# Optimization experiments

Hardware: AMD Instinct MI355X
Metric: run time of the kernel (lower is better)

## Reference

```python
import jax, jax.numpy as jnp
import numpy as np

D = 256  # atom_feature_dim
LN_EPS = 1e-5
NEG_SLOPE = 0.01  # LeakyReLU default


def setup_inputs() -> dict:
    key = jax.random.key(0)
    ks = jax.random.split(key, 8)
    B, N, L = 16, 256, 1024
    inv = 1.0 / np.sqrt(D)
    return {
        "mol_atom_feature": jax.random.normal(ks[0], (B, N, D), jnp.float32),
        "atom_feature": jax.random.normal(ks[1], (B, L, D), jnp.float32),
        "mol_atom_attend_mask": jnp.ones((B, L), jnp.float32),
        "mol_atom_softmax_mask": jnp.zeros((B, L), jnp.float32),
        # nn.Linear(D, D) params (weight stored [out, in] torch-style; we use x @ W.T form via einsum)
        "W_mol": jax.random.uniform(ks[2], (D, D), jnp.float32, -inv, inv),
        "b_mol": jnp.zeros((D,), jnp.float32),
        "W_nb": jax.random.uniform(ks[3], (D, D), jnp.float32, -inv, inv),
        "b_nb": jnp.zeros((D,), jnp.float32),
        # nn.Linear(2D, 1): weight [2D], bias scalar
        "align_w": jax.random.uniform(ks[4], (2 * D,), jnp.float32, -1.0 / np.sqrt(2 * D), 1.0 / np.sqrt(2 * D)),
        "align_b": jnp.zeros((), jnp.float32),
        "ln_gamma": jnp.ones((D,), jnp.float32),
        "ln_beta": jnp.zeros((D,), jnp.float32),
    }


def reference(mol_atom_feature, atom_feature, mol_atom_attend_mask, mol_atom_softmax_mask,
              W_mol, b_mol, W_nb, b_nb, align_w, align_b, ln_gamma, ln_beta):
    # Linear transforms (dropout is identity in eval)
    x = jnp.einsum('bnd,ed->bne', mol_atom_feature, W_mol) + b_mol   # [B,N,D]
    a = jnp.einsum('bld,ed->ble', atom_feature, W_nb) + b_nb        # [B,L,D]

    # GAT align: Linear over concat([x_i, a_j]) is separable:
    # score[b,n,l] = x[b,n]@w1 + a[b,l]@w2 + b
    w1, w2 = align_w[:D], align_w[D:]
    score = (x @ w1)[:, :, None] + (a @ w2)[:, None, :] + align_b   # [B,N,L]
    score = jax.nn.leaky_relu(score, NEG_SLOPE)

    # additive softmax mask over atom axis, then masked softmax + attend mask
    score = score + mol_atom_softmax_mask[:, None, :]
    attn = jax.nn.softmax(score, axis=-1)
    attn = attn * mol_atom_attend_mask[:, None, :]

    # weighted aggregation of transformed atom features
    ctx = jnp.einsum('bnl,bld->bnd', attn, a)                        # [B,N,D]

    # LayerNorm
    mu = jnp.mean(ctx, axis=-1, keepdims=True)
    var = jnp.var(ctx, axis=-1, keepdims=True)
    out = (ctx - mu) * jax.lax.rsqrt(var + LN_EPS) * ln_gamma + ln_beta
    return out
```

## Files before the change

### kernel.cpp

```cpp
#include <hip/hip_runtime.h>
#include <hip/hip_bf16.h>
#include <math.h>

#define BB 16
#define NN 256
#define LL 1024
#define DD 256

constexpr float LN_EPS = 1e-5f;
constexpr float NEG_SLOPE = 0.01f;

typedef __attribute__((ext_vector_type(8))) short short8;
typedef __attribute__((ext_vector_type(4))) float f32x4;
typedef __attribute__((ext_vector_type(4))) int i32x4;

static __device__ __forceinline__ unsigned cvtpk(float lo, float hi) {
  __hip_bfloat162 h = __float22bfloat162_rn(make_float2(lo, hi));
  union { __hip_bfloat162 h; unsigned u; } v; v.h = h;
  return v.u;
}
static __device__ __forceinline__ short8 pack8(float4 f0, float4 f1) {
  union { i32x4 i; short8 s; } v;
  v.i.x = cvtpk(f0.x, f0.y);
  v.i.y = cvtpk(f0.z, f0.w);
  v.i.z = cvtpk(f1.x, f1.y);
  v.i.w = cvtpk(f1.z, f1.w);
  return v.s;
}
static __device__ __forceinline__ unsigned short f2bf(float f) {
  union { float f; unsigned u; } v; v.f = f;
  unsigned r = v.u + 0x7FFFu + ((v.u >> 16) & 1u);
  return (unsigned short)(r >> 16);
}
static __device__ __forceinline__ float bf2f(unsigned short u) {
  union { unsigned u; float f; } v; v.u = ((unsigned)u) << 16;
  return v.f;
}

__global__ __launch_bounds__(512) void agemm_kernel(
    const float* __restrict__ atom, const float* __restrict__ W_nb,
    const float* __restrict__ b_nb, const float* __restrict__ W_mol,
    const float* __restrict__ b_mol, const float* __restrict__ align_w,
    const float* __restrict__ align_b, unsigned short* __restrict__ aT,
    float* __restrict__ s2, float* __restrict__ v1c) {
  __shared__ char atile[64 * 256 * 2];
  __shared__ unsigned short sAT[256 * 68];
  __shared__ float vp[32][16];

  int t = threadIdx.x;
  int w = t >> 6, lane = t & 63;
  int i = blockIdx.x;
  int x = i & 7, k = i >> 3;
  int b = x + 8 * (k >> 4);
  int l0 = (k & 15) * 64;
  int lo16 = lane & 15, g = lane >> 4;

  {
    int r = t >> 3, dseg = (t & 7) * 32;
    const float* src = atom + (size_t)(b * LL + l0 + r) * DD + dseg;
    #pragma unroll
    for (int q = 0; q < 4; ++q) {
      float4 f0 = *(const float4*)(src + q * 8);
      float4 f1 = *(const float4*)(src + q * 8 + 4);
      int byte = ((r * 256 + dseg + q * 8) * 2) ^ ((r & 7) << 4);
      *(short8*)(atile + byte) = pack8(f0, f1);
    }
  }

  if (i < 16) {
    int d0 = i * 16;
    int dl = t & 15, eseg = t >> 4;
    float acc = 0.f;
    #pragma unroll
    for (int q = 0; q < 8; ++q) {
      int e = eseg * 8 + q;
      acc += align_w[e] * W_mol[e * DD + d0 + dl];
    }
    vp[eseg][dl] = acc;
    __syncthreads();
    if (t < 16) {
      float s = 0.f;
      #pragma unroll
      for (int q = 0; q < 32; ++q) s += vp[q][t];
      v1c[d0 + t] = s;
    }
    if (i == 0 && w == 1) {
      float s = b_mol[lane] * align_w[lane] +
                b_mol[lane + 64] * align_w[lane + 64] +
                b_mol[lane + 128] * align_w[lane + 128] +
                b_mol[lane + 192] * align_w[lane + 192];
      #pragma unroll
      for (int off = 32; off > 0; off >>= 1) s += __shfl_xor(s, off, 64);
      if (lane == 0) v1c[256] = s + align_b[0];
    }
  }
  __syncthreads();

  f32x4 acc[2][4];
  #pragma unroll
  for (int m = 0; m < 2; ++m)
    #pragma unroll
    for (int n = 0; n < 4; ++n) acc[m][n] = f32x4{0.f, 0.f, 0.f, 0.f};

  const float* Ap = W_nb + (size_t)(w * 32 + lo16) * DD + g * 8;

  #pragma unroll 2
  for (int kk = 0; kk < 8; ++kk) {
    short8 af[2];
    #pragma unroll
    for (int m = 0; m < 2; ++m) {
      float4 f0 = *(const float4*)(Ap + m * 16 * DD + kk * 32);
      float4 f1 = *(const float4*)(Ap + m * 16 * DD + kk * 32 + 4);
      af[m] = pack8(f0, f1);
    }
    short8 bf[4];
    #pragma unroll
    for (int n = 0; n < 4; ++n) {
      int l = n * 16 + lo16;
      int byte = ((l * 256 + kk * 32 + g * 8) * 2) ^ ((l & 7) << 4);
      bf[n] = *(const short8*)(atile + byte);
    }
    #pragma unroll
    for (int m = 0; m < 2; ++m)
      #pragma unroll
      for (int n = 0; n < 4; ++n)
        acc[m][n] = __builtin_amdgcn_mfma_f32_16x16x32_bf16(af[m], bf[n],
                                                            acc[m][n], 0, 0, 0);
  }

  #pragma unroll
  for (int m = 0; m < 2; ++m) {
    int e_lo = w * 32 + m * 16 + g * 4;
    float4 bias = *(const float4*)&b_nb[e_lo];
    #pragma unroll
    for (int n = 0; n < 4; ++n) {
      int l = n * 16 + lo16;
      #pragma unroll
      for (int j = 0; j < 4; ++j) {
        float v = acc[m][n][j] + ((const float*)&bias)[j];
        sAT[(e_lo + j) * 68 + l] = f2bf(v);
      }
    }
  }
  __syncthreads();

  {
    int l = t >> 3, ech = (t & 7) * 32;
    float s = 0.f;
    #pragma unroll 8
    for (int q = 0; q < 32; ++q) {
      int e = ech + q;
      s += align_w[DD + e] * bf2f(sAT[e * 68 + l]);
    }
    s += __shfl_xor(s, 1, 64);
    s += __shfl_xor(s, 2, 64);
    s += __shfl_xor(s, 4, 64);
    if ((t & 7) == 0) s2[b * LL + l0 + l] = s;
  }

  unsigned short* dst = aT + (size_t)b * DD * LL + l0;
  #pragma unroll
  for (int idx = t; idx < 4096; idx += 512) {
    int e = idx >> 4, ch = idx & 15;
    ushort4 v = *(const ushort4*)&sAT[e * 68 + ch * 4];
    *(ushort4*)(dst + (size_t)e * LL + ch * 4) = v;
  }
}

__global__ __launch_bounds__(512) void attn_kernel(
    const unsigned short* __restrict__ aT, const float* __restrict__ mol,
    const float* __restrict__ v1c, const float* __restrict__ s2,
    const float* __restrict__ amask, const float* __restrict__ smask,
    const float* __restrict__ gamma, const float* __restrict__ beta,
    float* __restrict__ out) {
  __shared__ unsigned short sattn[16 * 1024];
  __shared__ float ctxp[2][16][DD];
  __shared__ float v1s[256];
  __shared__ float s1s[16];
  __shared__ float mu_s[16], rs_s[16];
  int i = blockIdx.x;
  int x = i & 7, k = i >> 3;
  int b = x + 8 * (k >> 4);
  int n0 = (k & 15) * 16;
  int t = threadIdx.x, w = t >> 6, lane = t & 63;

  float c0 = v1c[256];
  if (t < 256) v1s[t] = v1c[t];
  __syncthreads();

  {
    int r = t >> 5, off = (t & 31) * 8;
    const float* mr = mol + (size_t)(b * NN + n0 + r) * DD + off;
    float s = 0.f;
    #pragma unroll
    for (int q = 0; q < 2; ++q) {
      float4 f = *(const float4*)(mr + q * 4);
      s += f.x * v1s[off + q * 4] + f.y * v1s[off + q * 4 + 1] +
           f.z * v1s[off + q * 4 + 2] + f.w * v1s[off + q * 4 + 3];
    }
    s += __shfl_xor(s, 1, 64);
    s += __shfl_xor(s, 2, 64);
    s += __shfl_xor(s, 4, 64);
    s += __shfl_xor(s, 8, 64);
    s += __shfl_xor(s, 16, 64);
    if ((t & 31) == 0) s1s[r] = s + c0;
  }
  __syncthreads();

  {
    float s2v[16], amv[16], smv[16];
    #pragma unroll
    for (int q = 0; q < 16; ++q) {
      int l = lane + 64 * q;
      s2v[q] = s2[b * LL + l];
      amv[q] = amask[b * LL + l];
      smv[q] = smask[b * LL + l];
    }
    #pragma unroll
    for (int rr = 0; rr < 2; ++rr) {
      int r = w * 2 + rr;
      float s1v = s1s[r];
      float p[16];
      float mx = -INFINITY;
      #pragma unroll
      for (int q = 0; q < 16; ++q) {
        float sc = s1v + s2v[q];
        sc = sc > 0.f ? sc : NEG_SLOPE * sc;
        sc += smv[q];
        p[q] = sc;
        mx = fmaxf(mx, sc);
      }
      #pragma unroll
      for (int off = 32; off > 0; off >>= 1) mx = fmaxf(mx, __shfl_xor(mx, off, 64));
      float sum = 0.f;
      #pragma unroll
      for (int q = 0; q < 16; ++q) {
        p[q] = __expf(p[q] - mx);
        sum += p[q];
      }
      #pragma unroll
      for (int off = 32; off > 0; off >>= 1) sum += __shfl_xor(sum, off, 64);
      float inv = 1.f / sum;
      #pragma unroll
      for (int q = 0; q < 16; ++q) {
        unsigned short bv = f2bf(p[q] * amv[q] * inv);
        int l = lane + 64 * q;
        int byte = ((r * 1024 + l) * 2) ^ ((r & 7) << 4);
        *(unsigned short*)((char*)sattn + byte) = bv;
      }
    }
  }
  __syncthreads();

  int lo16 = lane & 15, g = lane >> 4;
  int e0 = (w & 3) * 64, lh = w >> 2;
  f32x4 acc[4];
  #pragma unroll
  for (int n = 0; n < 4; ++n) acc[n] = f32x4{0.f, 0.f, 0.f, 0.f};
  const unsigned short* Bp =
      aT + (size_t)b * DD * LL + (size_t)(e0 + lo16) * LL + lh * 512 + g * 8;
  #pragma unroll 4
  for (int kk = 0; kk < 16; ++kk) {
    short8 afr = *(const short8*)((const char*)sattn +
        (((lo16 * 1024 + lh * 512 + kk * 32 + g * 8) * 2) ^ ((lo16 & 7) << 4)));
    #pragma unroll
    for (int n = 0; n < 4; ++n) {
      short8 bfr = *(const short8*)(Bp + (size_t)n * 16 * LL + kk * 32);
      acc[n] = __builtin_amdgcn_mfma_f32_16x16x32_bf16(afr, bfr, acc[n], 0, 0, 0);
    }
  }
  #pragma unroll
  for (int n = 0; n < 4; ++n)
    #pragma unroll
    for (int j = 0; j < 4; ++j)
      ctxp[lh][g * 4 + j][e0 + n * 16 + lo16] = acc[n][j];
  __syncthreads();

  #pragma unroll
  for (int rr = 0; rr < 2; ++rr) {
    int r = w * 2 + rr;
    float s = 0.f, sq = 0.f;
    #pragma unroll
    for (int jj = 0; jj < 4; ++jj) {
      int cc = lane + 64 * jj;
      float v = ctxp[0][r][cc] + ctxp[1][r][cc];
      s += v;
      sq += v * v;
    }
    #pragma unroll
    for (int off = 32; off > 0; off >>= 1) {
      s += __shfl_xor(s, off, 64);
      sq += __shfl_xor(sq, off, 64);
    }
    if (lane == 0) {
      float mu = s * (1.f / 256.f);
      float var = sq * (1.f / 256.f) - mu * mu;
      mu_s[r] = mu;
      rs_s[r] = rsqrtf(var + LN_EPS);
    }
  }
  __syncthreads();

  #pragma unroll
  for (int q = 0; q < 8; ++q) {
    int idx = t + 512 * q;
    int r = idx >> 8, d = idx & 255;
    float v = ctxp[0][r][d] + ctxp[1][r][d];
    out[(size_t)(b * NN + n0 + r) * DD + d] =
        (v - mu_s[r]) * rs_s[r] * gamma[d] + beta[d];
  }
}

extern "C" void kernel_launch(void* const* d_in, const int* in_sizes, int n_in,
                              void* d_out, int out_size, void* d_ws, size_t ws_size,
                              hipStream_t stream) {
  const float* mol     = (const float*)d_in[0];
  const float* atom    = (const float*)d_in[1];
  const float* amask   = (const float*)d_in[2];
  const float* smask   = (const float*)d_in[3];
  const float* W_mol   = (const float*)d_in[4];
  const float* b_mol   = (const float*)d_in[5];
  const float* W_nb    = (const float*)d_in[6];
  const float* b_nb    = (const float*)d_in[7];
  const float* align_w = (const float*)d_in[8];
  const float* align_b = (const float*)d_in[9];
  const float* gamma   = (const float*)d_in[10];
  const float* beta    = (const float*)d_in[11];
  float* outp = (float*)d_out;

  char* wsb = (char*)d_ws;
  unsigned short* aT = (unsigned short*)wsb;
  float* s2  = (float*)(wsb + 8388608);
  float* v1c = s2 + BB * LL;

  agemm_kernel<<<256, 512, 0, stream>>>(atom, W_nb, b_nb, W_mol, b_mol,
                                        align_w, align_b, aT, s2, v1c);
  attn_kernel<<<256, 512, 0, stream>>>(aT, mol, v1c, s2, amask, smask,
                                       gamma, beta, outp);
}
```

Before: 40.79 us.

## Double threads per block to 1024 and redistribute work in both kernels

Both kernels now launch 1024 threads (16 waves) per block instead of 512. Each wave handles half as much work: in the GEMM each wave owns one 16-row M tile, and in the attention kernel each wave owns one softmax row and a quarter of the L reduction, with four partial ctx buffers summed afterwards. The goal is more waves per CU to hide memory latency on a grid of only 256 blocks. In exchange, shared memory grows for ctxp, the partial sums need an extra reduction step, and per-thread register limits get tighter.

Result: slower. 41.66 us (+2.1%).

```diff
diff --git a/kernel.cpp b/kernel.cpp
--- a/kernel.cpp
+++ b/kernel.cpp
@@ -37,7 +37,7 @@
   return v.f;
 }
 
-__global__ __launch_bounds__(512) void agemm_kernel(
+__global__ __launch_bounds__(1024) void agemm_kernel(
     const float* __restrict__ atom, const float* __restrict__ W_nb,
     const float* __restrict__ b_nb, const float* __restrict__ W_mol,
     const float* __restrict__ b_mol, const float* __restrict__ align_w,
@@ -45,7 +45,7 @@
     float* __restrict__ s2, float* __restrict__ v1c) {
   __shared__ char atile[64 * 256 * 2];
   __shared__ unsigned short sAT[256 * 68];
-  __shared__ float vp[32][16];
+  __shared__ float vp[64][16];
 
   int t = threadIdx.x;
   int w = t >> 6, lane = t & 63;
@@ -56,10 +56,10 @@
   int lo16 = lane & 15, g = lane >> 4;
 
   {
-    int r = t >> 3, dseg = (t & 7) * 32;
+    int r = t >> 4, dseg = (t & 15) * 16;
     const float* src = atom + (size_t)(b * LL + l0 + r) * DD + dseg;
     #pragma unroll
-    for (int q = 0; q < 4; ++q) {
+    for (int q = 0; q < 2; ++q) {
       float4 f0 = *(const float4*)(src + q * 8);
       float4 f1 = *(const float4*)(src + q * 8 + 4);
       int byte = ((r * 256 + dseg + q * 8) * 2) ^ ((r & 7) << 4);
@@ -72,8 +72,8 @@
     int dl = t & 15, eseg = t >> 4;
     float acc = 0.f;
     #pragma unroll
-    for (int q = 0; q < 8; ++q) {
-      int e = eseg * 8 + q;
+    for (int q = 0; q < 4; ++q) {
+      int e = eseg * 4 + q;
       acc += align_w[e] * W_mol[e * DD + d0 + dl];
     }
     vp[eseg][dl] = acc;
@@ -81,7 +81,7 @@
     if (t < 16) {
       float s = 0.f;
       #pragma unroll
-      for (int q = 0; q < 32; ++q) s += vp[q][t];
+      for (int q = 0; q < 64; ++q) s += vp[q][t];
       v1c[d0 + t] = s;
     }
     if (i == 0 && w == 1) {
@@ -96,48 +96,35 @@
   }
   __syncthreads();
 
-  f32x4 acc[2][4];
-  #pragma unroll
-  for (int m = 0; m < 2; ++m)
-    #pragma unroll
-    for (int n = 0; n < 4; ++n) acc[m][n] = f32x4{0.f, 0.f, 0.f, 0.f};
-
-  const float* Ap = W_nb + (size_t)(w * 32 + lo16) * DD + g * 8;
-
-  #pragma unroll 2
+  f32x4 acc[4];
+  #pragma unroll
+  for (int n = 0; n < 4; ++n) acc[n] = f32x4{0.f, 0.f, 0.f, 0.f};
+
+  const float* Ap = W_nb + (size_t)(w * 16 + lo16) * DD + g * 8;
+
+  #pragma unroll 4
   for (int kk = 0; kk < 8; ++kk) {
-    short8 af[2];
-    #pragma unroll
-    for (int m = 0; m < 2; ++m) {
-      float4 f0 = *(const float4*)(Ap + m * 16 * DD + kk * 32);
-      float4 f1 = *(const float4*)(Ap + m * 16 * DD + kk * 32 + 4);
-      af[m] = pack8(f0, f1);
-    }
-    short8 bf[4];
+    float4 f0 = *(const float4*)(Ap + kk * 32);
+    float4 f1 = *(const float4*)(Ap + kk * 32 + 4);
+    short8 af = pack8(f0, f1);
     #pragma unroll
     for (int n = 0; n < 4; ++n) {
       int l = n * 16 + lo16;
       int byte = ((l * 256 + kk * 32 + g * 8) * 2) ^ ((l & 7) << 4);
-      bf[n] = *(const short8*)(atile + byte);
-    }
-    #pragma unroll
-    for (int m = 0; m < 2; ++m)
-      #pragma unroll
-      for (int n = 0; n < 4; ++n)
-        acc[m][n] = __builtin_amdgcn_mfma_f32_16x16x32_bf16(af[m], bf[n],
-                                                            acc[m][n], 0, 0, 0);
-  }
-
-  #pragma unroll
-  for (int m = 0; m < 2; ++m) {
-    int e_lo = w * 32 + m * 16 + g * 4;
+      short8 bf = *(const short8*)(atile + byte);
+      acc[n] = __builtin_amdgcn_mfma_f32_16x16x32_bf16(af, bf, acc[n], 0, 0, 0);
+    }
+  }
+
+  {
+    int e_lo = w * 16 + g * 4;
     float4 bias = *(const float4*)&b_nb[e_lo];
     #pragma unroll
     for (int n = 0; n < 4; ++n) {
       int l = n * 16 + lo16;
       #pragma unroll
       for (int j = 0; j < 4; ++j) {
-        float v = acc[m][n][j] + ((const float*)&bias)[j];
+        float v = acc[n][j] + ((const float*)&bias)[j];
         sAT[(e_lo + j) * 68 + l] = f2bf(v);
       }
     }
@@ -145,36 +132,37 @@
   __syncthreads();
 
   {
-    int l = t >> 3, ech = (t & 7) * 32;
+    int l = t >> 4, ech = (t & 15) * 16;
     float s = 0.f;
     #pragma unroll 8
-    for (int q = 0; q < 32; ++q) {
+    for (int q = 0; q < 16; ++q) {
       int e = ech + q;
       s += align_w[DD + e] * bf2f(sAT[e * 68 + l]);
     }
     s += __shfl_xor(s, 1, 64);
     s += __shfl_xor(s, 2, 64);
     s += __shfl_xor(s, 4, 64);
-    if ((t & 7) == 0) s2[b * LL + l0 + l] = s;
+    s += __shfl_xor(s, 8, 64);
+    if ((t & 15) == 0) s2[b * LL + l0 + l] = s;
   }
 
   unsigned short* dst = aT + (size_t)b * DD * LL + l0;
   #pragma unroll
-  for (int idx = t; idx < 4096; idx += 512) {
+  for (int idx = t; idx < 4096; idx += 1024) {
     int e = idx >> 4, ch = idx & 15;
     ushort4 v = *(const ushort4*)&sAT[e * 68 + ch * 4];
     *(ushort4*)(dst + (size_t)e * LL + ch * 4) = v;
   }
 }
 
-__global__ __launch_bounds__(512) void attn_kernel(
+__global__ __launch_bounds__(1024) void attn_kernel(
     const unsigned short* __restrict__ aT, const float* __restrict__ mol,
     const float* __restrict__ v1c, const float* __restrict__ s2,
     const float* __restrict__ amask, const float* __restrict__ smask,
     const float* __restrict__ gamma, const float* __restrict__ beta,
     float* __restrict__ out) {
   __shared__ unsigned short sattn[16 * 1024];
-  __shared__ float ctxp[2][16][DD];
+  __shared__ float ctxp[4][16][DD];
   __shared__ float v1s[256];
   __shared__ float s1s[16];
   __shared__ float mu_s[16], rs_s[16];
@@ -189,80 +177,63 @@
   __syncthreads();
 
   {
-    int r = t >> 5, off = (t & 31) * 8;
-    const float* mr = mol + (size_t)(b * NN + n0 + r) * DD + off;
-    float s = 0.f;
-    #pragma unroll
-    for (int q = 0; q < 2; ++q) {
-      float4 f = *(const float4*)(mr + q * 4);
-      s += f.x * v1s[off + q * 4] + f.y * v1s[off + q * 4 + 1] +
-           f.z * v1s[off + q * 4 + 2] + f.w * v1s[off + q * 4 + 3];
-    }
-    s += __shfl_xor(s, 1, 64);
-    s += __shfl_xor(s, 2, 64);
-    s += __shfl_xor(s, 4, 64);
-    s += __shfl_xor(s, 8, 64);
-    s += __shfl_xor(s, 16, 64);
-    if ((t & 31) == 0) s1s[r] = s + c0;
-  }
-  __syncthreads();
-
-  {
-    float s2v[16], amv[16], smv[16];
+    const float* mr = mol + (size_t)(b * NN + n0 + w) * DD + lane * 4;
+    float4 f = *(const float4*)mr;
+    float s = f.x * v1s[lane * 4] + f.y * v1s[lane * 4 + 1] +
+              f.z * v1s[lane * 4 + 2] + f.w * v1s[lane * 4 + 3];
+    #pragma unroll
+    for (int off = 32; off > 0; off >>= 1) s += __shfl_xor(s, off, 64);
+    if (lane == 0) s1s[w] = s + c0;
+  }
+  __syncthreads();
+
+  {
+    int r = w;
+    float s1v = s1s[r];
+    float p[16], amv[16];
+    float mx = -INFINITY;
     #pragma unroll
     for (int q = 0; q < 16; ++q) {
       int l = lane + 64 * q;
-      s2v[q] = s2[b * LL + l];
+      float sc = s1v + s2[b * LL + l];
+      sc = sc > 0.f ? sc : NEG_SLOPE * sc;
+      sc += smask[b * LL + l];
       amv[q] = amask[b * LL + l];
-      smv[q] = smask[b * LL + l];
-    }
-    #pragma unroll
-    for (int rr = 0; rr < 2; ++rr) {
-      int r = w * 2 + rr;
-      float s1v = s1s[r];
-      float p[16];
-      float mx = -INFINITY;
-      #pragma unroll
-      for (int q = 0; q < 16; ++q) {
-        float sc = s1v + s2v[q];
-        sc = sc > 0.f ? sc : NEG_SLOPE * sc;
-        sc += smv[q];
-        p[q] = sc;
-        mx = fmaxf(mx, sc);
-      }
-      #pragma unroll
-      for (int off = 32; off > 0; off >>= 1) mx = fmaxf(mx, __shfl_xor(mx, off, 64));
-      float sum = 0.f;
-      #pragma unroll
-      for (int q = 0; q < 16; ++q) {
-        p[q] = __expf(p[q] - mx);
-        sum += p[q];
-      }
-      #pragma unroll
-      for (int off = 32; off > 0; off >>= 1) sum += __shfl_xor(sum, off, 64);
-      float inv = 1.f / sum;
-      #pragma unroll
-      for (int q = 0; q < 16; ++q) {
-        unsigned short bv = f2bf(p[q] * amv[q] * inv);
-        int l = lane + 64 * q;
-        int byte = ((r * 1024 + l) * 2) ^ ((r & 7) << 4);
-        *(unsigned short*)((char*)sattn + byte) = bv;
-      }
+      p[q] = sc;
+      mx = fmaxf(mx, sc);
+    }
+    #pragma unroll
+    for (int off = 32; off > 0; off >>= 1) mx = fmaxf(mx, __shfl_xor(mx, off, 64));
+    float sum = 0.f;
+    #pragma unroll
+    for (int q = 0; q < 16; ++q) {
+      p[q] = __expf(p[q] - mx);
+      sum += p[q];
+    }
+    #pragma unroll
+    for (int off = 32; off > 0; off >>= 1) sum += __shfl_xor(sum, off, 64);
+    float inv = 1.f / sum;
+    #pragma unroll
+    for (int q = 0; q < 16; ++q) {
+      unsigned short bv = f2bf(p[q] * amv[q] * inv);
+      int l = lane + 64 * q;
+      int byte = ((r * 1024 + l) * 2) ^ ((r & 7) << 4);
+      *(unsigned short*)((char*)sattn + byte) = bv;
     }
   }
   __syncthreads();
 
   int lo16 = lane & 15, g = lane >> 4;
-  int e0 = (w & 3) * 64, lh = w >> 2;
+  int e0 = (w & 3) * 64, lq = w >> 2;
   f32x4 acc[4];
   #pragma unroll
   for (int n = 0; n < 4; ++n) acc[n] = f32x4{0.f, 0.f, 0.f, 0.f};
   const unsigned short* Bp =
-      aT + (size_t)b * DD * LL + (size_t)(e0 + lo16) * LL + lh * 512 + g * 8;
+      aT + (size_t)b * DD * LL + (size_t)(e0 + lo16) * LL + lq * 256 + g * 8;
   #pragma unroll 4
-  for (int kk = 0; kk < 16; ++kk) {
+  for (int kk = 0; kk < 8; ++kk) {
     short8 afr = *(const short8*)((const char*)sattn +
-        (((lo16 * 1024 + lh * 512 + kk * 32 + g * 8) * 2) ^ ((lo16 & 7) << 4)));
+        (((lo16 * 1024 + lq * 256 + kk * 32 + g * 8) * 2) ^ ((lo16 & 7) << 4)));
     #pragma unroll
     for (int n = 0; n < 4; ++n) {
       short8 bfr = *(const short8*)(Bp + (size_t)n * 16 * LL + kk * 32);
@@ -273,17 +244,16 @@
   for (int n = 0; n < 4; ++n)
     #pragma unroll
     for (int j = 0; j < 4; ++j)
-      ctxp[lh][g * 4 + j][e0 + n * 16 + lo16] = acc[n][j];
-  __syncthreads();
-
-  #pragma unroll
-  for (int rr = 0; rr < 2; ++rr) {
-    int r = w * 2 + rr;
+      ctxp[lq][g * 4 + j][e0 + n * 16 + lo16] = acc[n][j];
+  __syncthreads();
+
+  {
+    int r = w;
     float s = 0.f, sq = 0.f;
     #pragma unroll
     for (int jj = 0; jj < 4; ++jj) {
       int cc = lane + 64 * jj;
-      float v = ctxp[0][r][cc] + ctxp[1][r][cc];
+      float v = ctxp[0][r][cc] + ctxp[1][r][cc] + ctxp[2][r][cc] + ctxp[3][r][cc];
       s += v;
       sq += v * v;
     }
@@ -302,10 +272,10 @@
   __syncthreads();
 
   #pragma unroll
-  for (int q = 0; q < 8; ++q) {
-    int idx = t + 512 * q;
+  for (int q = 0; q < 4; ++q) {
+    int idx = t + 1024 * q;
     int r = idx >> 8, d = idx & 255;
-    float v = ctxp[0][r][d] + ctxp[1][r][d];
+    float v = ctxp[0][r][d] + ctxp[1][r][d] + ctxp[2][r][d] + ctxp[3][r][d];
     out[(size_t)(b * NN + n0 + r) * DD + d] =
         (v - mu_s[r]) * rs_s[r] * gamma[d] + beta[d];
   }
@@ -333,8 +303,8 @@
   float* s2  = (float*)(wsb + 8388608);
   float* v1c = s2 + BB * LL;
 
-  agemm_kernel<<<256, 512, 0, stream>>>(atom, W_nb, b_nb, W_mol, b_mol,
-                                        align_w, align_b, aT, s2, v1c);
-  attn_kernel<<<256, 512, 0, stream>>>(aT, mol, v1c, s2, amask, smask,
-                                       gamma, beta, outp);
-}
+  agemm_kernel<<<256, 1024, 0, stream>>>(atom, W_nb, b_nb, W_mol, b_mol,
+                                         align_w, align_b, aT, s2, v1c);
+  attn_kernel<<<256, 1024, 0, stream>>>(aT, mol, v1c, s2, amask, smask,
+                                        gamma, beta, outp);
+}
```

## Halve agemm tile to double grid, fuse s2 dot into epilogue, recompute s1 via MFMA

Applied to the files above, without the earlier changes.

The first kernel now processes 32 atoms per block instead of 64, doubling the grid to 512 blocks and shrinking shared memory. The align dot product for s2 is folded into the MFMA epilogue using full-precision values and shuffles, rather than a second pass over the bf16 staging buffer. The W_mol·align_w folding is removed. Each attention block instead recomputes x = mol·W_molᵀ for its 16 rows with MFMA and reduces it against align_w, which adds per-block GEMM work and W_mol reads but drops the serial dependency.

New measurement: 55.22 us. 1.35x slower.

```diff
diff --git a/kernel.cpp b/kernel.cpp
--- a/kernel.cpp
+++ b/kernel.cpp
@@ -32,150 +32,119 @@
   unsigned r = v.u + 0x7FFFu + ((v.u >> 16) & 1u);
   return (unsigned short)(r >> 16);
 }
-static __device__ __forceinline__ float bf2f(unsigned short u) {
-  union { unsigned u; float f; } v; v.u = ((unsigned)u) << 16;
-  return v.f;
-}
-
-__global__ __launch_bounds__(512) void agemm_kernel(
+
+__global__ __launch_bounds__(512, 4) void agemm_kernel(
     const float* __restrict__ atom, const float* __restrict__ W_nb,
-    const float* __restrict__ b_nb, const float* __restrict__ W_mol,
-    const float* __restrict__ b_mol, const float* __restrict__ align_w,
-    const float* __restrict__ align_b, unsigned short* __restrict__ aT,
-    float* __restrict__ s2, float* __restrict__ v1c) {
-  __shared__ char atile[64 * 256 * 2];
-  __shared__ unsigned short sAT[256 * 68];
-  __shared__ float vp[32][16];
-
-  int t = threadIdx.x;
-  int w = t >> 6, lane = t & 63;
+    const float* __restrict__ b_nb, const float* __restrict__ align_w,
+    unsigned short* __restrict__ aT, float* __restrict__ s2g) {
+  __shared__ char atile[32 * 256 * 2];
+  __shared__ unsigned short sAT[256 * 40];
+  __shared__ float s2p[8][32];
+
+  int t = threadIdx.x, w = t >> 6, lane = t & 63;
+  int lo16 = lane & 15, g = lane >> 4;
   int i = blockIdx.x;
   int x = i & 7, k = i >> 3;
-  int b = x + 8 * (k >> 4);
-  int l0 = (k & 15) * 64;
-  int lo16 = lane & 15, g = lane >> 4;
+  int b = x + 8 * (k >> 5);
+  int l0 = (k & 31) * 32;
 
   {
-    int r = t >> 3, dseg = (t & 7) * 32;
+    int r = t >> 4, dseg = (t & 15) * 16;
     const float* src = atom + (size_t)(b * LL + l0 + r) * DD + dseg;
     #pragma unroll
-    for (int q = 0; q < 4; ++q) {
+    for (int q = 0; q < 2; ++q) {
       float4 f0 = *(const float4*)(src + q * 8);
       float4 f1 = *(const float4*)(src + q * 8 + 4);
       int byte = ((r * 256 + dseg + q * 8) * 2) ^ ((r & 7) << 4);
       *(short8*)(atile + byte) = pack8(f0, f1);
     }
   }
-
-  if (i < 16) {
-    int d0 = i * 16;
-    int dl = t & 15, eseg = t >> 4;
-    float acc = 0.f;
-    #pragma unroll
-    for (int q = 0; q < 8; ++q) {
-      int e = eseg * 8 + q;
-      acc += align_w[e] * W_mol[e * DD + d0 + dl];
-    }
-    vp[eseg][dl] = acc;
-    __syncthreads();
-    if (t < 16) {
-      float s = 0.f;
-      #pragma unroll
-      for (int q = 0; q < 32; ++q) s += vp[q][t];
-      v1c[d0 + t] = s;
-    }
-    if (i == 0 && w == 1) {
-      float s = b_mol[lane] * align_w[lane] +
-                b_mol[lane + 64] * align_w[lane + 64] +
-                b_mol[lane + 128] * align_w[lane + 128] +
-                b_mol[lane + 192] * align_w[lane + 192];
-      #pragma unroll
-      for (int off = 32; off > 0; off >>= 1) s += __shfl_xor(s, off, 64);
-      if (lane == 0) v1c[256] = s + align_b[0];
-    }
-  }
-  __syncthreads();
-
-  f32x4 acc[2][4];
-  #pragma unroll
-  for (int m = 0; m < 2; ++m)
-    #pragma unroll
-    for (int n = 0; n < 4; ++n) acc[m][n] = f32x4{0.f, 0.f, 0.f, 0.f};
+  __syncthreads();
+
+  f32x4 acc[2][2];
+  #pragma unroll
+  for (int eg = 0; eg < 2; ++eg)
+    #pragma unroll
+    for (int lg = 0; lg < 2; ++lg) acc[eg][lg] = f32x4{0.f, 0.f, 0.f, 0.f};
 
   const float* Ap = W_nb + (size_t)(w * 32 + lo16) * DD + g * 8;
-
   #pragma unroll 2
   for (int kk = 0; kk < 8; ++kk) {
-    short8 af[2];
-    #pragma unroll
-    for (int m = 0; m < 2; ++m) {
-      float4 f0 = *(const float4*)(Ap + m * 16 * DD + kk * 32);
-      float4 f1 = *(const float4*)(Ap + m * 16 * DD + kk * 32 + 4);
-      af[m] = pack8(f0, f1);
-    }
-    short8 bf[4];
-    #pragma unroll
-    for (int n = 0; n < 4; ++n) {
-      int l = n * 16 + lo16;
+    short8 afk[2];
+    #pragma unroll
+    for (int eg = 0; eg < 2; ++eg) {
+      float4 f0 = *(const float4*)(Ap + eg * 16 * DD + kk * 32);
+      float4 f1 = *(const float4*)(Ap + eg * 16 * DD + kk * 32 + 4);
+      afk[eg] = pack8(f0, f1);
+    }
+    short8 bfa[2];
+    #pragma unroll
+    for (int lg = 0; lg < 2; ++lg) {
+      int l = lg * 16 + lo16;
       int byte = ((l * 256 + kk * 32 + g * 8) * 2) ^ ((l & 7) << 4);
-      bf[n] = *(const short8*)(atile + byte);
-    }
-    #pragma unroll
-    for (int m = 0; m < 2; ++m)
-      #pragma unroll
-      for (int n = 0; n < 4; ++n)
-        acc[m][n] = __builtin_amdgcn_mfma_f32_16x16x32_bf16(af[m], bf[n],
-                                                            acc[m][n], 0, 0, 0);
-  }
-
-  #pragma unroll
-  for (int m = 0; m < 2; ++m) {
-    int e_lo = w * 32 + m * 16 + g * 4;
-    float4 bias = *(const float4*)&b_nb[e_lo];
-    #pragma unroll
-    for (int n = 0; n < 4; ++n) {
-      int l = n * 16 + lo16;
-      #pragma unroll
-      for (int j = 0; j < 4; ++j) {
-        float v = acc[m][n][j] + ((const float*)&bias)[j];
-        sAT[(e_lo + j) * 68 + l] = f2bf(v);
-      }
-    }
-  }
-  __syncthreads();
-
-  {
-    int l = t >> 3, ech = (t & 7) * 32;
+      bfa[lg] = *(const short8*)(atile + byte);
+    }
+    #pragma unroll
+    for (int eg = 0; eg < 2; ++eg)
+      #pragma unroll
+      for (int lg = 0; lg < 2; ++lg)
+        acc[eg][lg] = __builtin_amdgcn_mfma_f32_16x16x32_bf16(
+            afk[eg], bfa[lg], acc[eg][lg], 0, 0, 0);
+  }
+
+  float4 bias[2], w2r[2];
+  #pragma unroll
+  for (int eg = 0; eg < 2; ++eg) {
+    bias[eg] = *(const float4*)&b_nb[w * 32 + eg * 16 + g * 4];
+    w2r[eg] = *(const float4*)&align_w[DD + w * 32 + eg * 16 + g * 4];
+  }
+  float p0 = 0.f, p1 = 0.f;
+  #pragma unroll
+  for (int eg = 0; eg < 2; ++eg) {
+    #pragma unroll
+    for (int jj = 0; jj < 4; ++jj) {
+      int e = w * 32 + eg * 16 + g * 4 + jj;
+      float v0 = acc[eg][0][jj] + ((const float*)&bias[eg])[jj];
+      float v1 = acc[eg][1][jj] + ((const float*)&bias[eg])[jj];
+      sAT[e * 40 + lo16] = f2bf(v0);
+      sAT[e * 40 + 16 + lo16] = f2bf(v1);
+      p0 += ((const float*)&w2r[eg])[jj] * v0;
+      p1 += ((const float*)&w2r[eg])[jj] * v1;
+    }
+  }
+  p0 += __shfl_xor(p0, 16, 64); p0 += __shfl_xor(p0, 32, 64);
+  p1 += __shfl_xor(p1, 16, 64); p1 += __shfl_xor(p1, 32, 64);
+  if (g == 0) {
+    s2p[w][lo16] = p0;
+    s2p[w][16 + lo16] = p1;
+  }
+  __syncthreads();
+
+  if (t < 32) {
     float s = 0.f;
-    #pragma unroll 8
-    for (int q = 0; q < 32; ++q) {
-      int e = ech + q;
-      s += align_w[DD + e] * bf2f(sAT[e * 68 + l]);
-    }
-    s += __shfl_xor(s, 1, 64);
-    s += __shfl_xor(s, 2, 64);
-    s += __shfl_xor(s, 4, 64);
-    if ((t & 7) == 0) s2[b * LL + l0 + l] = s;
-  }
-
+    #pragma unroll
+    for (int q = 0; q < 8; ++q) s += s2p[q][t];
+    s2g[b * LL + l0 + t] = s;
+  }
   unsigned short* dst = aT + (size_t)b * DD * LL + l0;
   #pragma unroll
-  for (int idx = t; idx < 4096; idx += 512) {
-    int e = idx >> 4, ch = idx & 15;
-    ushort4 v = *(const ushort4*)&sAT[e * 68 + ch * 4];
+  for (int idx = t; idx < 2048; idx += 512) {
+    int e = idx >> 3, ch = idx & 7;
+    ushort4 v = *(const ushort4*)&sAT[e * 40 + ch * 4];
     *(ushort4*)(dst + (size_t)e * LL + ch * 4) = v;
   }
 }
 
 __global__ __launch_bounds__(512) void attn_kernel(
     const unsigned short* __restrict__ aT, const float* __restrict__ mol,
-    const float* __restrict__ v1c, const float* __restrict__ s2,
-    const float* __restrict__ amask, const float* __restrict__ smask,
-    const float* __restrict__ gamma, const float* __restrict__ beta,
-    float* __restrict__ out) {
+    const float* __restrict__ W_mol, const float* __restrict__ b_mol,
+    const float* __restrict__ align_w, const float* __restrict__ align_b,
+    const float* __restrict__ s2g, const float* __restrict__ amask,
+    const float* __restrict__ smask, const float* __restrict__ gamma,
+    const float* __restrict__ beta, float* __restrict__ out) {
   __shared__ unsigned short sattn[16 * 1024];
   __shared__ float ctxp[2][16][DD];
-  __shared__ float v1s[256];
+  __shared__ float s1p[8][16];
   __shared__ float s1s[16];
   __shared__ float mu_s[16], rs_s[16];
   int i = blockIdx.x;
@@ -183,27 +152,52 @@
   int b = x + 8 * (k >> 4);
   int n0 = (k & 15) * 16;
   int t = threadIdx.x, w = t >> 6, lane = t & 63;
-
-  float c0 = v1c[256];
-  if (t < 256) v1s[t] = v1c[t];
-  __syncthreads();
+  int lo16 = lane & 15, g = lane >> 4;
 
   {
-    int r = t >> 5, off = (t & 31) * 8;
-    const float* mr = mol + (size_t)(b * NN + n0 + r) * DD + off;
-    float s = 0.f;
-    #pragma unroll
-    for (int q = 0; q < 2; ++q) {
-      float4 f = *(const float4*)(mr + q * 4);
-      s += f.x * v1s[off + q * 4] + f.y * v1s[off + q * 4 + 1] +
-           f.z * v1s[off + q * 4 + 2] + f.w * v1s[off + q * 4 + 3];
-    }
-    s += __shfl_xor(s, 1, 64);
-    s += __shfl_xor(s, 2, 64);
-    s += __shfl_xor(s, 4, 64);
-    s += __shfl_xor(s, 8, 64);
-    s += __shfl_xor(s, 16, 64);
-    if ((t & 31) == 0) s1s[r] = s + c0;
+    f32x4 accx[2];
+    accx[0] = f32x4{0.f, 0.f, 0.f, 0.f};
+    accx[1] = f32x4{0.f, 0.f, 0.f, 0.f};
+    const float* molp = mol + (size_t)(b * NN + n0 + lo16) * DD + g * 8;
+    const float* wmp = W_mol + (size_t)(w * 32 + lo16) * DD + g * 8;
+    #pragma unroll 2
+    for (int kk = 0; kk < 8; ++kk) {
+      float4 m0 = *(const float4*)(molp + kk * 32);
+      float4 m1 = *(const float4*)(molp + kk * 32 + 4);
+      short8 afm = pack8(m0, m1);
+      #pragma unroll
+      for (int eg = 0; eg < 2; ++eg) {
+        float4 f0 = *(const float4*)(wmp + eg * 16 * DD + kk * 32);
+        float4 f1 = *(const float4*)(wmp + eg * 16 * DD + kk * 32 + 4);
+        short8 bfw = pack8(f0, f1);
+        accx[eg] = __builtin_amdgcn_mfma_f32_16x16x32_bf16(afm, bfw,
+                                                           accx[eg], 0, 0, 0);
+      }
+    }
+    float q4[4] = {0.f, 0.f, 0.f, 0.f};
+    #pragma unroll
+    for (int eg = 0; eg < 2; ++eg) {
+      int e = w * 32 + eg * 16 + lo16;
+      float w1v = align_w[e], bmv = b_mol[e];
+      #pragma unroll
+      for (int jj = 0; jj < 4; ++jj) q4[jj] += w1v * (accx[eg][jj] + bmv);
+    }
+    #pragma unroll
+    for (int m = 1; m <= 8; m <<= 1) {
+      #pragma unroll
+      for (int jj = 0; jj < 4; ++jj) q4[jj] += __shfl_xor(q4[jj], m, 64);
+    }
+    if (lo16 == 0) {
+      #pragma unroll
+      for (int jj = 0; jj < 4; ++jj) s1p[w][g * 4 + jj] = q4[jj];
+    }
+  }
+  __syncthreads();
+  if (t < 16) {
+    float s = align_b[0];
+    #pragma unroll
+    for (int q = 0; q < 8; ++q) s += s1p[q][t];
+    s1s[t] = s;
   }
   __syncthreads();
 
@@ -212,7 +206,7 @@
     #pragma unroll
     for (int q = 0; q < 16; ++q) {
       int l = lane + 64 * q;
-      s2v[q] = s2[b * LL + l];
+      s2v[q] = s2g[b * LL + l];
       amv[q] = amask[b * LL + l];
       smv[q] = smask[b * LL + l];
     }
@@ -252,28 +246,29 @@
   }
   __syncthreads();
 
-  int lo16 = lane & 15, g = lane >> 4;
-  int e0 = (w & 3) * 64, lh = w >> 2;
-  f32x4 acc[4];
-  #pragma unroll
-  for (int n = 0; n < 4; ++n) acc[n] = f32x4{0.f, 0.f, 0.f, 0.f};
-  const unsigned short* Bp =
-      aT + (size_t)b * DD * LL + (size_t)(e0 + lo16) * LL + lh * 512 + g * 8;
-  #pragma unroll 4
-  for (int kk = 0; kk < 16; ++kk) {
-    short8 afr = *(const short8*)((const char*)sattn +
-        (((lo16 * 1024 + lh * 512 + kk * 32 + g * 8) * 2) ^ ((lo16 & 7) << 4)));
-    #pragma unroll
-    for (int n = 0; n < 4; ++n) {
-      short8 bfr = *(const short8*)(Bp + (size_t)n * 16 * LL + kk * 32);
-      acc[n] = __builtin_amdgcn_mfma_f32_16x16x32_bf16(afr, bfr, acc[n], 0, 0, 0);
-    }
-  }
-  #pragma unroll
-  for (int n = 0; n < 4; ++n)
-    #pragma unroll
-    for (int j = 0; j < 4; ++j)
-      ctxp[lh][g * 4 + j][e0 + n * 16 + lo16] = acc[n][j];
+  {
+    int e0 = (w & 3) * 64, lh = w >> 2;
+    f32x4 acc[4];
+    #pragma unroll
+    for (int n = 0; n < 4; ++n) acc[n] = f32x4{0.f, 0.f, 0.f, 0.f};
+    const unsigned short* Bp =
+        aT + (size_t)b * DD * LL + (size_t)(e0 + lo16) * LL + lh * 512 + g * 8;
+    #pragma unroll 4
+    for (int kk = 0; kk < 16; ++kk) {
+      short8 afr = *(const short8*)((const char*)sattn +
+          (((lo16 * 1024 + lh * 512 + kk * 32 + g * 8) * 2) ^ ((lo16 & 7) << 4)));
+      #pragma unroll
+      for (int n = 0; n < 4; ++n) {
+        short8 bfr = *(const short8*)(Bp + (size_t)n * 16 * LL + kk * 32);
+        acc[n] = __builtin_amdgcn_mfma_f32_16x16x32_bf16(afr, bfr, acc[n], 0, 0, 0);
+      }
+    }
+    #pragma unroll
+    for (int n = 0; n < 4; ++n)
+      #pragma unroll
+      for (int jj = 0; jj < 4; ++jj)
+        ctxp[lh][g * 4 + jj][e0 + n * 16 + lo16] = acc[n][jj];
+  }
   __syncthreads();
 
   #pragma unroll
@@ -330,11 +325,10 @@
 
   char* wsb = (char*)d_ws;
   unsigned short* aT = (unsigned short*)wsb;
-  float* s2  = (float*)(wsb + 8388608);
-  float* v1c = s2 + BB * LL;
-
-  agemm_kernel<<<256, 512, 0, stream>>>(atom, W_nb, b_nb, W_mol, b_mol,
-                                        align_w, align_b, aT, s2, v1c);
-  attn_kernel<<<256, 512, 0, stream>>>(aT, mol, v1c, s2, amask, smask,
-                                       gamma, beta, outp);
-}
+  float* s2g = (float*)(wsb + 8388608);
+
+  agemm_kernel<<<512, 512, 0, stream>>>(atom, W_nb, b_nb, align_w, aT, s2g);
+  attn_kernel<<<256, 512, 0, stream>>>(aT, mol, W_mol, b_mol, align_w,
+                                       align_b, s2g, amask, smask, gamma,
+                                       beta, outp);
+}
```

## Fuse s2 projection into GEMM epilogue and stage masks in shared memory

Applied to the files above, without the earlier changes.

The agemm kernel's warp tiling changes from 32 e-rows x 64 l to 64 e-rows x 32 l per wave. The a·w2 dot product (s2) is now computed from fp32 accumulators in the epilogue, with shuffle and shared-memory reductions. This removes a separate pass that reread bf16 sAT from LDS and also makes s2 come from unrounded values. The attn kernel now loads s2, the attend mask and the softmax mask once into shared memory with float4 loads instead of holding 48 strided scalar loads in registers, which reduces register pressure at the cost of extra LDS reads.

Measured after the change: 46.79 us. 14.7% more time.

```diff
diff --git a/kernel.cpp b/kernel.cpp
--- a/kernel.cpp
+++ b/kernel.cpp
@@ -32,20 +32,17 @@
   unsigned r = v.u + 0x7FFFu + ((v.u >> 16) & 1u);
   return (unsigned short)(r >> 16);
 }
-static __device__ __forceinline__ float bf2f(unsigned short u) {
-  union { unsigned u; float f; } v; v.u = ((unsigned)u) << 16;
-  return v.f;
-}
 
 __global__ __launch_bounds__(512) void agemm_kernel(
     const float* __restrict__ atom, const float* __restrict__ W_nb,
     const float* __restrict__ b_nb, const float* __restrict__ W_mol,
     const float* __restrict__ b_mol, const float* __restrict__ align_w,
     const float* __restrict__ align_b, unsigned short* __restrict__ aT,
-    float* __restrict__ s2, float* __restrict__ v1c) {
+    float* __restrict__ s2g, float* __restrict__ v1c) {
   __shared__ char atile[64 * 256 * 2];
   __shared__ unsigned short sAT[256 * 68];
   __shared__ float vp[32][16];
+  __shared__ float s2p[8][34];
 
   int t = threadIdx.x;
   int w = t >> 6, lane = t & 63;
@@ -96,68 +93,80 @@
   }
   __syncthreads();
 
-  f32x4 acc[2][4];
+  int e0 = (w & 3) * 64;
+  int lsub = (w >> 2) * 32;
+
+  f32x4 acc[4][2];
   #pragma unroll
-  for (int m = 0; m < 2; ++m)
-    #pragma unroll
-    for (int n = 0; n < 4; ++n) acc[m][n] = f32x4{0.f, 0.f, 0.f, 0.f};
-
-  const float* Ap = W_nb + (size_t)(w * 32 + lo16) * DD + g * 8;
+  for (int m = 0; m < 4; ++m)
+    #pragma unroll
+    for (int n = 0; n < 2; ++n) acc[m][n] = f32x4{0.f, 0.f, 0.f, 0.f};
+
+  const float* Ap = W_nb + (size_t)(e0 + lo16) * DD + g * 8;
 
   #pragma unroll 2
   for (int kk = 0; kk < 8; ++kk) {
-    short8 af[2];
-    #pragma unroll
-    for (int m = 0; m < 2; ++m) {
+    short8 af[4];
+    #pragma unroll
+    for (int m = 0; m < 4; ++m) {
       float4 f0 = *(const float4*)(Ap + m * 16 * DD + kk * 32);
       float4 f1 = *(const float4*)(Ap + m * 16 * DD + kk * 32 + 4);
       af[m] = pack8(f0, f1);
     }
-    short8 bf[4];
-    #pragma unroll
-    for (int n = 0; n < 4; ++n) {
-      int l = n * 16 + lo16;
+    short8 bf[2];
+    #pragma unroll
+    for (int n = 0; n < 2; ++n) {
+      int l = lsub + n * 16 + lo16;
       int byte = ((l * 256 + kk * 32 + g * 8) * 2) ^ ((l & 7) << 4);
       bf[n] = *(const short8*)(atile + byte);
     }
     #pragma unroll
-    for (int m = 0; m < 2; ++m)
-      #pragma unroll
-      for (int n = 0; n < 4; ++n)
+    for (int m = 0; m < 4; ++m)
+      #pragma unroll
+      for (int n = 0; n < 2; ++n)
         acc[m][n] = __builtin_amdgcn_mfma_f32_16x16x32_bf16(af[m], bf[n],
                                                             acc[m][n], 0, 0, 0);
   }
 
-  #pragma unroll
-  for (int m = 0; m < 2; ++m) {
-    int e_lo = w * 32 + m * 16 + g * 4;
-    float4 bias = *(const float4*)&b_nb[e_lo];
-    #pragma unroll
-    for (int n = 0; n < 4; ++n) {
-      int l = n * 16 + lo16;
-      #pragma unroll
-      for (int j = 0; j < 4; ++j) {
-        float v = acc[m][n][j] + ((const float*)&bias)[j];
-        sAT[(e_lo + j) * 68 + l] = f2bf(v);
-      }
-    }
-  }
-  __syncthreads();
-
-  {
-    int l = t >> 3, ech = (t & 7) * 32;
-    float s = 0.f;
-    #pragma unroll 8
-    for (int q = 0; q < 32; ++q) {
-      int e = ech + q;
-      s += align_w[DD + e] * bf2f(sAT[e * 68 + l]);
-    }
-    s += __shfl_xor(s, 1, 64);
-    s += __shfl_xor(s, 2, 64);
-    s += __shfl_xor(s, 4, 64);
-    if ((t & 7) == 0) s2[b * LL + l0 + l] = s;
-  }
-
+  {
+    float4 bias[4], w2r[4];
+    #pragma unroll
+    for (int m = 0; m < 4; ++m) {
+      bias[m] = *(const float4*)&b_nb[e0 + m * 16 + g * 4];
+      w2r[m] = *(const float4*)&align_w[DD + e0 + m * 16 + g * 4];
+    }
+    float p[2] = {0.f, 0.f};
+    #pragma unroll
+    for (int m = 0; m < 4; ++m) {
+      #pragma unroll
+      for (int n = 0; n < 2; ++n) {
+        int l = lsub + n * 16 + lo16;
+        #pragma unroll
+        for (int jj = 0; jj < 4; ++jj) {
+          float v = acc[m][n][jj] + ((const float*)&bias[m])[jj];
+          sAT[(e0 + m * 16 + g * 4 + jj) * 68 + l] = f2bf(v);
+          p[n] += ((const float*)&w2r[m])[jj] * v;
+        }
+      }
+    }
+    #pragma unroll
+    for (int n = 0; n < 2; ++n) {
+      p[n] += __shfl_xor(p[n], 16, 64);
+      p[n] += __shfl_xor(p[n], 32, 64);
+    }
+    if (g == 0) {
+      s2p[w][lo16] = p[0];
+      s2p[w][16 + lo16] = p[1];
+    }
+  }
+  __syncthreads();
+
+  if (t < 64) {
+    int wh = (t >> 5) * 4;
+    int li = t & 31;
+    float s = s2p[wh][li] + s2p[wh + 1][li] + s2p[wh + 2][li] + s2p[wh + 3][li];
+    s2g[b * LL + l0 + t] = s;
+  }
   unsigned short* dst = aT + (size_t)b * DD * LL + l0;
   #pragma unroll
   for (int idx = t; idx < 4096; idx += 512) {
@@ -169,12 +178,13 @@
 
 __global__ __launch_bounds__(512) void attn_kernel(
     const unsigned short* __restrict__ aT, const float* __restrict__ mol,
-    const float* __restrict__ v1c, const float* __restrict__ s2,
+    const float* __restrict__ v1c, const float* __restrict__ s2g,
     const float* __restrict__ amask, const float* __restrict__ smask,
     const float* __restrict__ gamma, const float* __restrict__ beta,
     float* __restrict__ out) {
   __shared__ unsigned short sattn[16 * 1024];
   __shared__ float ctxp[2][16][DD];
+  __shared__ float s2_s[LL], am_s[LL], sm_s[LL];
   __shared__ float v1s[256];
   __shared__ float s1s[16];
   __shared__ float mu_s[16], rs_s[16];
@@ -186,6 +196,15 @@
 
   float c0 = v1c[256];
   if (t < 256) v1s[t] = v1c[t];
+  if (t < 256) {
+    *(float4*)&s2_s[t * 4] = *(const float4*)&s2g[b * LL + t * 4];
+  } else {
+    int u = t - 256;
+    *(float4*)&am_s[u * 4] = *(const float4*)&amask[b * LL + u * 4];
+  }
+  if (t < 256) {
+    *(float4*)&sm_s[t * 4] = *(const float4*)&smask[b * LL + t * 4];
+  }
   __syncthreads();
 
   {
@@ -208,14 +227,6 @@
   __syncthreads();
 
   {
-    float s2v[16], amv[16], smv[16];
-    #pragma unroll
-    for (int q = 0; q < 16; ++q) {
-      int l = lane + 64 * q;
-      s2v[q] = s2[b * LL + l];
-      amv[q] = amask[b * LL + l];
-      smv[q] = smask[b * LL + l];
-    }
     #pragma unroll
     for (int rr = 0; rr < 2; ++rr) {
       int r = w * 2 + rr;
@@ -224,9 +235,10 @@
       float mx = -INFINITY;
       #pragma unroll
       for (int q = 0; q < 16; ++q) {
-        float sc = s1v + s2v[q];
+        int l = lane + 64 * q;
+        float sc = s1v + s2_s[l];
         sc = sc > 0.f ? sc : NEG_SLOPE * sc;
-        sc += smv[q];
+        sc += sm_s[l];
         p[q] = sc;
         mx = fmaxf(mx, sc);
       }
@@ -243,8 +255,8 @@
       float inv = 1.f / sum;
       #pragma unroll
       for (int q = 0; q < 16; ++q) {
-        unsigned short bv = f2bf(p[q] * amv[q] * inv);
         int l = lane + 64 * q;
+        unsigned short bv = f2bf(p[q] * am_s[l] * inv);
         int byte = ((r * 1024 + l) * 2) ^ ((r & 7) << 4);
         *(unsigned short*)((char*)sattn + byte) = bv;
       }
@@ -253,27 +265,29 @@
   __syncthreads();
 
   int lo16 = lane & 15, g = lane >> 4;
-  int e0 = (w & 3) * 64, lh = w >> 2;
-  f32x4 acc[4];
-  #pragma unroll
-  for (int n = 0; n < 4; ++n) acc[n] = f32x4{0.f, 0.f, 0.f, 0.f};
-  const unsigned short* Bp =
-      aT + (size_t)b * DD * LL + (size_t)(e0 + lo16) * LL + lh * 512 + g * 8;
-  #pragma unroll 4
-  for (int kk = 0; kk < 16; ++kk) {
-    short8 afr = *(const short8*)((const char*)sattn +
-        (((lo16 * 1024 + lh * 512 + kk * 32 + g * 8) * 2) ^ ((lo16 & 7) << 4)));
-    #pragma unroll
-    for (int n = 0; n < 4; ++n) {
-      short8 bfr = *(const short8*)(Bp + (size_t)n * 16 * LL + kk * 32);
-      acc[n] = __builtin_amdgcn_mfma_f32_16x16x32_bf16(afr, bfr, acc[n], 0, 0, 0);
-    }
-  }
-  #pragma unroll
-  for (int n = 0; n < 4; ++n)
-    #pragma unroll
-    for (int j = 0; j < 4; ++j)
-      ctxp[lh][g * 4 + j][e0 + n * 16 + lo16] = acc[n][j];
+  {
+    int e0 = (w & 3) * 64, lh = w >> 2;
+    f32x4 acc[4];
+    #pragma unroll
+    for (int n = 0; n < 4; ++n) acc[n] = f32x4{0.f, 0.f, 0.f, 0.f};
+    const unsigned short* Bp =
+        aT + (size_t)b * DD * LL + (size_t)(e0 + lo16) * LL + lh * 512 + g * 8;
+    #pragma unroll 4
+    for (int kk = 0; kk < 16; ++kk) {
+      short8 afr = *(const short8*)((const char*)sattn +
+          (((lo16 * 1024 + lh * 512 + kk * 32 + g * 8) * 2) ^ ((lo16 & 7) << 4)));
+      #pragma unroll
+      for (int n = 0; n < 4; ++n) {
+        short8 bfr = *(const short8*)(Bp + (size_t)n * 16 * LL + kk * 32);
+        acc[n] = __builtin_amdgcn_mfma_f32_16x16x32_bf16(afr, bfr, acc[n], 0, 0, 0);
+      }
+    }
+    #pragma unroll
+    for (int n = 0; n < 4; ++n)
+      #pragma unroll
+      for (int jj = 0; jj < 4; ++jj)
+        ctxp[lh][g * 4 + jj][e0 + n * 16 + lo16] = acc[n][jj];
+  }
   __syncthreads();
 
   #pragma unroll
@@ -330,11 +344,11 @@
 
   char* wsb = (char*)d_ws;
   unsigned short* aT = (unsigned short*)wsb;
-  float* s2  = (float*)(wsb + 8388608);
-  float* v1c = s2 + BB * LL;
+  float* s2g = (float*)(wsb + 8388608);
+  float* v1c = s2g + BB * LL;
 
   agemm_kernel<<<256, 512, 0, stream>>>(atom, W_nb, b_nb, W_mol, b_mol,
-                                        align_w, align_b, aT, s2, v1c);
-  attn_kernel<<<256, 512, 0, stream>>>(aT, mol, v1c, s2, amask, smask,
+                                        align_w, align_b, aT, s2g, v1c);
+  attn_kernel<<<256, 512, 0, stream>>>(aT, mol, v1c, s2g, amask, smask,
                                        gamma, beta, outp);
 }
```
